# Kernel tuning notes

Measured on AMD Instinct MI355X. Metric: run time of the kernel, lower is better.

Reference implementation:

```python
import jax, jax.numpy as jnp
import numpy as np

B, S, H, M, E = 64, 512, 1024, 26, 676  # batch, seq, hidden, max_nodes, max_edges (M*M)


def setup_inputs() -> dict:
    key = jax.random.key(0)
    ks = jax.random.split(key, 16)
    seq = jax.random.normal(ks[0], (B, S, H), jnp.float32)
    # ragged, strictly-increasing sentence-end offsets in [1, S-1], zero-padded tail
    rng = np.random.RandomState(0)
    off = np.zeros((B, M - 1), np.int64)
    for b in range(B):
        c = rng.randint(5, M)  # count of valid offsets per sample (ragged)
        off[b, :c] = np.sort(rng.choice(np.arange(1, S), size=c, replace=False))
    s = 1.0 / np.sqrt(H)
    s3 = 1.0 / np.sqrt(3 * H)
    return {
        'sequence_outputs': seq,
        'proof_offsets': jnp.asarray(off),
        'node_labels': jax.random.randint(ks[1], (B, M), 0, 2),
        'edge_labels': jax.random.randint(ks[2], (B, E), 0, 2),
        'W_naf': jax.random.normal(ks[3], (H, H), jnp.float32) * s,
        'b_naf': jnp.zeros((H,), jnp.float32),
        'W_cd': jax.random.normal(ks[4], (H, H), jnp.float32) * s,
        'b_cd': jnp.zeros((H,), jnp.float32),
        'W_co': jax.random.normal(ks[5], (H, 2), jnp.float32) * s,
        'b_co': jnp.zeros((2,), jnp.float32),
        'W_nd': jax.random.normal(ks[6], (H, H), jnp.float32) * s,
        'b_nd': jnp.zeros((H,), jnp.float32),
        'W_no': jax.random.normal(ks[7], (H, 2), jnp.float32) * s,
        'b_no': jnp.zeros((2,), jnp.float32),
        'W_ed': jax.random.normal(ks[8], (3 * H, H), jnp.float32) * s3,
        'b_ed': jnp.zeros((H,), jnp.float32),
        'W_eo': jax.random.normal(ks[9], (H, 2), jnp.float32) * s,
        'b_eo': jnp.zeros((2,), jnp.float32),
    }


def reference(sequence_outputs, proof_offsets, node_labels, edge_labels,
              W_naf, b_naf, W_cd, b_cd, W_co, b_co,
              W_nd, b_nd, W_no, b_no, W_ed, b_ed, W_eo, b_eo):
    Bx, Sx, Hx = sequence_outputs.shape
    Mx = node_labels.shape[1]
    Ex = edge_labels.shape[1]

    cls = sequence_outputs[:, 0, :]                       # [B,H]
    naf = cls @ W_naf + b_naf                             # NAF node embedding
    logits = jnp.tanh(cls @ W_cd + b_cd) @ W_co + b_co    # RobertaClassificationHead (eval: dropout=id)

    # segment-mean pooling via inclusive prefix sums: segment j = tokens (prev_j, off_j]
    P = jnp.cumsum(sequence_outputs, axis=1)              # [B,S,H]
    off = proof_offsets                                   # [B,M-1]
    prev = jnp.concatenate([jnp.zeros((Bx, 1), off.dtype), off[:, :-1]], axis=1)
    valid = off > 0                                       # [B,M-1]
    seg_sum = (jnp.take_along_axis(P, off[..., None], axis=1)
               - jnp.take_along_axis(P, prev[..., None], axis=1))  # [B,M-1,H]
    seg_len = jnp.maximum(off - prev, 1).astype(sequence_outputs.dtype)
    seg_mean = seg_sum / seg_len[..., None] * valid[..., None]

    count = valid.sum(axis=1)                             # nodes per sample (excl. NAF)
    # node embeddings: seg means at 0..count-1, NAF at index count, zeros after
    node_full = jnp.concatenate([seg_mean, jnp.zeros((Bx, 1, Hx), seg_mean.dtype)], axis=1)  # [B,M,H]
    idx = jnp.arange(Mx)
    node_full = node_full + (idx[None, :, None] == count[:, None, None]) * naf[:, None, :]

    # all-pairs edge features over n=count+1 nodes, row-major flat k=i*n+j, zero-padded to E
    n = count + 1                                         # [B]
    k = jnp.arange(Ex)                                    # [E]
    i = jnp.clip(k[None, :] // n[:, None], 0, Mx - 1)     # [B,E]
    j = jnp.clip(k[None, :] % n[:, None], 0, Mx - 1)
    valid_e = (k[None, :] < (n * n)[:, None])[..., None]
    ni = jnp.take_along_axis(node_full, i[..., None], axis=1)  # [B,E,H]
    nj = jnp.take_along_axis(node_full, j[..., None], axis=1)
    edge = jnp.concatenate([nj, ni, nj - ni], axis=-1) * valid_e  # [B,E,3H]

    node_logits = jnp.tanh(node_full @ W_nd + b_nd) @ W_no + b_no
    edge_logits = jnp.tanh(edge @ W_ed + b_ed) @ W_eo + b_eo
    return (logits, node_logits, edge_logits)
```

## Files before the change

### kernel.cpp

```cpp
#include <hip/hip_runtime.h>
#include <hip/hip_bf16.h>

#define B_ 64
#define S_ 512
#define H_ 1024
#define M_ 26
#define E_ 676

typedef short bf16x8 __attribute__((ext_vector_type(8)));
typedef float f32x4 __attribute__((ext_vector_type(4)));

__device__ __forceinline__ void gload16(const void* g, void* l) {
    __builtin_amdgcn_global_load_lds((const __attribute__((address_space(1))) unsigned int*)g,
                                     (__attribute__((address_space(3))) unsigned int*)l,
                                     16, 0, 0);
}

__device__ __forceinline__ float tanh_fast(float x) {
    float e = __expf(2.0f * x);
    return 1.0f - 2.0f * __builtin_amdgcn_rcpf(e + 1.0f);
}

__global__ __launch_bounds__(256) void k_seg(
    const float* __restrict__ seq, const int* __restrict__ off,
    float* __restrict__ node_sum) {
    __shared__ float rows[8 * 1024];
    __shared__ int offs[26];
    __shared__ int cs[2];
    int bid = blockIdx.x;
    int tid = threadIdx.x;
    int chunk = bid & 63, b = bid >> 6;
    int t0 = chunk * 8;
    int wid = tid >> 6;

    const float* sq = seq + (size_t)b * S_ * H_ + (size_t)t0 * H_ + tid * 4;
    float* ld = rows + wid * 256;
#pragma unroll
    for (int i = 0; i < 8; ++i)
        gload16(sq + i * H_, ld + i * 1024);

    if (tid < M_ - 1) offs[tid] = off[b * (M_ - 1) + tid];
    __syncthreads();
    if (tid == 0) {
        int c = 0;
        while (c < M_ - 1 && offs[c] > 0) c++;
        cs[0] = c; cs[1] = (c > 0) ? offs[c - 1] : 0;
    }
    __syncthreads();
    int c = cs[0], offmax = cs[1];
    int ts = max(t0, 1), te = min(t0 + 7, offmax);
    if (ts > te) return;
    int m = 0;
    while (m < c && offs[m] < ts) m++;
    float4 acc = make_float4(0, 0, 0, 0);
#pragma unroll
    for (int i = 0; i < 8; ++i) {
        int t = t0 + i;
        if (t < ts || t > te) continue;
        if (offs[m] < t) {
            float* dst = node_sum + ((size_t)(b * M_ + m)) * H_ + tid * 4;
            atomicAdd(dst + 0, acc.x); atomicAdd(dst + 1, acc.y);
            atomicAdd(dst + 2, acc.z); atomicAdd(dst + 3, acc.w);
            acc = make_float4(0, 0, 0, 0);
            while (offs[m] < t) m++;
        }
        float4 v = *(const float4*)(rows + i * 1024 + tid * 4);
        acc.x += v.x; acc.y += v.y; acc.z += v.z; acc.w += v.w;
    }
    float* dst = node_sum + ((size_t)(b * M_ + m)) * H_ + tid * 4;
    atomicAdd(dst + 0, acc.x); atomicAdd(dst + 1, acc.y);
    atomicAdd(dst + 2, acc.z); atomicAdd(dst + 3, acc.w);
}

__global__ __launch_bounds__(256) void k_stage1b(
    const float* __restrict__ seq, const int* __restrict__ off,
    const float* __restrict__ Wnaf, const float* __restrict__ Wcd,
    const float* __restrict__ Wnd, const float* __restrict__ Wed,
    const float* __restrict__ bed, const float* __restrict__ Weo,
    const float* __restrict__ beo,
    __hip_bfloat16* __restrict__ Wt, int* __restrict__ count,
    float* __restrict__ econ, float* __restrict__ naf, float* __restrict__ cdh) {
    __shared__ float smem[2048];
    int bid = blockIdx.x;
    int tid = threadIdx.x;

    if (bid < 256) {
        float (*As)[64] = (float(*)[64])smem;
        float (*Bs)[64] = (float(*)[64])(smem + 1024);
        int e = bid;
        int bx = e & 31;
        int kbase = (e >> 5) * 128;
        const float* W;
        float* dst;
        int cbase;
        if (bx < 16) { W = Wnaf; dst = naf; cbase = bx * 64; }
        else         { W = Wcd;  dst = cdh; cbase = (bx - 16) * 64; }
        int tx = tid % 16, ty = tid / 16;
        float c[4][4] = {};
        int la_row = tid / 4;
        int la_k4  = (tid % 4) * 4;
        int lb_k   = tid / 16;
        int lb_c4  = (tid % 16) * 4;
        for (int k0 = 0; k0 < 128; k0 += 16) {
            float4 a = *(const float4*)(seq + (size_t)la_row * S_ * H_ + kbase + k0 + la_k4);
            *(float4*)(&Bs[lb_k][lb_c4]) =
                *(const float4*)(W + (size_t)(kbase + k0 + lb_k) * H_ + cbase + lb_c4);
            As[la_k4 + 0][la_row] = a.x;
            As[la_k4 + 1][la_row] = a.y;
            As[la_k4 + 2][la_row] = a.z;
            As[la_k4 + 3][la_row] = a.w;
            __syncthreads();
#pragma unroll
            for (int kk = 0; kk < 16; ++kk) {
                float4 av = *(const float4*)(&As[kk][ty * 4]);
                float4 bv = *(const float4*)(&Bs[kk][tx * 4]);
                c[0][0] += av.x * bv.x; c[0][1] += av.x * bv.y; c[0][2] += av.x * bv.z; c[0][3] += av.x * bv.w;
                c[1][0] += av.y * bv.x; c[1][1] += av.y * bv.y; c[1][2] += av.y * bv.z; c[1][3] += av.y * bv.w;
                c[2][0] += av.z * bv.x; c[2][1] += av.z * bv.y; c[2][2] += av.z * bv.z; c[2][3] += av.z * bv.w;
                c[3][0] += av.w * bv.x; c[3][1] += av.w * bv.y; c[3][2] += av.w * bv.z; c[3][3] += av.w * bv.w;
            }
            __syncthreads();
        }
#pragma unroll
        for (int i = 0; i < 4; ++i)
#pragma unroll
            for (int j = 0; j < 4; ++j)
                atomicAdd(dst + (size_t)(ty * 4 + i) * H_ + cbase + tx * 4 + j, c[i][j]);
    } else if (bid < 3328) {
        float (*T)[33] = (float(*)[33])smem;
        int idx = bid - 256;
        int s = idx >> 10, rem = idx & 1023;
        int bx = rem & 31, by = rem >> 5;
        int c = tid & 31, r0 = tid >> 5;
        const int HH = H_ * H_;
#pragma unroll
        for (int i = 0; i < 4; ++i) {
            int r = r0 + 8 * i;
            size_t k = by * 32 + r, n = bx * 32 + c;
            float v;
            if (s == 0)      v = Wnd[k * H_ + n];
            else if (s == 1) v = Wed[k * H_ + n] + Wed[2 * HH + k * H_ + n];
            else             v = Wed[HH + k * H_ + n] - Wed[2 * HH + k * H_ + n];
            T[r][c] = v;
        }
        __syncthreads();
#pragma unroll
        for (int i = 0; i < 4; ++i) {
            int rr = r0 + 8 * i;
            Wt[(size_t)(s * H_ + bx * 32 + rr) * H_ + by * 32 + c] = __float2bfloat16(T[c][rr]);
        }
    } else if (bid == 3328) {
        if (tid < 64) {
            int b = tid;
            int c = 0;
            for (int m = 0; m < M_ - 1; ++m) c += (off[b * (M_ - 1) + m] > 0) ? 1 : 0;
            count[b] = c;
        }
    } else {
        float* s0 = smem; float* s1 = smem + 256;
        float a0 = 0.f, a1 = 0.f;
        for (int h = tid; h < H_; h += 256) {
            float t = tanh_fast(bed[h]);
            a0 += t * Weo[h * 2 + 0];
            a1 += t * Weo[h * 2 + 1];
        }
        s0[tid] = a0; s1[tid] = a1; __syncthreads();
        for (int o = 128; o > 0; o >>= 1) {
            if (tid < o) { s0[tid] += s0[tid + o]; s1[tid] += s1[tid + o]; }
            __syncthreads();
        }
        if (tid == 0) { econ[0] = s0[0] + beo[0]; econ[1] = s1[0] + beo[1]; }
    }
}

__global__ __launch_bounds__(256) void k_stage2(
    const float* __restrict__ sums, const int* __restrict__ off,
    const int* __restrict__ count, const float* __restrict__ naf,
    const float* __restrict__ bnaf, __hip_bfloat16* __restrict__ nodeB,
    const float* __restrict__ cdh, const float* __restrict__ bcd,
    const float* __restrict__ Wco, const float* __restrict__ bco,
    float* __restrict__ out) {
    __shared__ float smem[512];
    int bid = blockIdx.x;
    int tid = threadIdx.x;
    if (bid < 1664) {
        int b = bid / 26, m = bid - b * 26;
        int cnt = count[b];
        float4 v = make_float4(0, 0, 0, 0);
        const float4* row = (const float4*)(sums + ((size_t)(b * M_ + m)) * H_);
        if (m < M_ - 1) {
            int o = off[b * (M_ - 1) + m];
            if (o > 0) {
                int prev = (m > 0) ? off[b * (M_ - 1) + m - 1] : 0;
                float inv = 1.0f / (float)max(o - prev, 1);
                float4 s = row[tid];
                v = make_float4(s.x * inv, s.y * inv, s.z * inv, s.w * inv);
            }
        }
        if (m == cnt) {
            float4 a = ((const float4*)(naf + (size_t)b * H_))[tid];
            float4 bb = ((const float4*)bnaf)[tid];
            v.x += a.x + bb.x; v.y += a.y + bb.y; v.z += a.z + bb.z; v.w += a.w + bb.w;
        }
        __hip_bfloat16 __attribute__((aligned(8))) h[4] = {
            __float2bfloat16(v.x), __float2bfloat16(v.y),
            __float2bfloat16(v.z), __float2bfloat16(v.w)};
        *(ushort4*)(nodeB + ((size_t)(b * M_ + m)) * H_ + tid * 4) = *(const ushort4*)h;
    } else {
        int b = bid - 1664;
        float* s0 = smem; float* s1 = smem + 256;
        float a0 = 0.f, a1 = 0.f;
        for (int h = tid; h < H_; h += 256) {
            float t = tanh_fast(cdh[(size_t)b * H_ + h] + bcd[h]);
            a0 += t * Wco[h * 2 + 0];
            a1 += t * Wco[h * 2 + 1];
        }
        s0[tid] = a0; s1[tid] = a1; __syncthreads();
        for (int o = 128; o > 0; o >>= 1) {
            if (tid < o) { s0[tid] += s0[tid + o]; s1[tid] += s1[tid + o]; }
            __syncthreads();
        }
        if (tid == 0) { out[b * 2 + 0] = s0[0] + bco[0]; out[b * 2 + 1] = s1[0] + bco[1]; }
    }
}

#define GM 1664
#define GN 3072
#define GK 1024
__global__ __launch_bounds__(256) void k_mfma(const __hip_bfloat16* __restrict__ A,
                                              const __hip_bfloat16* __restrict__ Bt,
                                              float* __restrict__ C) {
    __shared__ __hip_bfloat16 As[128 * 32];
    __shared__ __hip_bfloat16 Bs[128 * 32];
    int tid = threadIdx.x;
    int wid = tid >> 6, ln = tid & 63;
    int row0 = blockIdx.y * 128, col0 = blockIdx.x * 128;
    const __hip_bfloat16* ga = A + (size_t)(row0 + wid * 16 + (ln >> 2)) * GK + (ln & 3) * 8;
    const __hip_bfloat16* gb = Bt + (size_t)(col0 + wid * 16 + (ln >> 2)) * GK + (ln & 3) * 8;
    __hip_bfloat16* lA = As + wid * 512;
    __hip_bfloat16* lB = Bs + wid * 512;
    int mrow = (wid >> 1) * 64, ncol = (wid & 1) * 64;
    int l15 = ln & 15, l4 = ln >> 4;
    f32x4 acc[4][4] = {};
    const __hip_bfloat16* pa = As + (size_t)(mrow + l15) * 32 + l4 * 8;
    const __hip_bfloat16* pb = Bs + (size_t)(ncol + l15) * 32 + l4 * 8;
    for (int k0 = 0; k0 < GK; k0 += 32) {
        gload16(ga, lA);
        gload16(ga + 64 * GK, lA + 2048);
        gload16(gb, lB);
        gload16(gb + 64 * GK, lB + 2048);
        ga += 32; gb += 32;
        __syncthreads();
        bf16x8 af[4], bf[4];
#pragma unroll
        for (int mi = 0; mi < 4; ++mi) af[mi] = *(const bf16x8*)(pa + mi * 16 * 32);
#pragma unroll
        for (int ni = 0; ni < 4; ++ni) bf[ni] = *(const bf16x8*)(pb + ni * 16 * 32);
#pragma unroll
        for (int mi = 0; mi < 4; ++mi)
#pragma unroll
            for (int ni = 0; ni < 4; ++ni)
                acc[mi][ni] = __builtin_amdgcn_mfma_f32_16x16x32_bf16(af[mi], bf[ni],
                                                                      acc[mi][ni], 0, 0, 0);
        __syncthreads();
    }
#pragma unroll
    for (int mi = 0; mi < 4; ++mi)
#pragma unroll
        for (int ni = 0; ni < 4; ++ni) {
            f32x4 v = acc[mi][ni];
            size_t r = row0 + mrow + mi * 16 + l4 * 4;
            size_t cc = col0 + ncol + ni * 16 + l15;
            C[(r + 0) * GN + cc] = v[0];
            C[(r + 1) * GN + cc] = v[1];
            C[(r + 2) * GN + cc] = v[2];
            C[(r + 3) * GN + cc] = v[3];
        }
}

__global__ __launch_bounds__(256) void k_stage4(
    const float* __restrict__ Cm, const int* __restrict__ count,
    const float* __restrict__ bnd, const float* __restrict__ Wno,
    const float* __restrict__ bno, const float* __restrict__ bed,
    const float* __restrict__ Weo, const float* __restrict__ beo,
    const float* __restrict__ econ, float* __restrict__ out_n,
    float* __restrict__ out_e) {
    int bid = blockIdx.x;
    int wid = threadIdx.x >> 6, lane = threadIdx.x & 63;
    if (bid < 416) {
        int r = bid * 4 + wid;
        const float4* src = (const float4*)(Cm + (size_t)r * GN);
        float a0 = 0.f, a1 = 0.f;
#pragma unroll
        for (int it = 0; it < 4; ++it) {
            int h = lane * 4 + it * 256;
            float4 s = src[lane + it * 64];
            float4 bb = *(const float4*)(bnd + h);
            float t0 = tanh_fast(s.x + bb.x), t1 = tanh_fast(s.y + bb.y);
            float t2 = tanh_fast(s.z + bb.z), t3 = tanh_fast(s.w + bb.w);
            a0 += t0 * Wno[h * 2 + 0] + t1 * Wno[h * 2 + 2] + t2 * Wno[h * 2 + 4] + t3 * Wno[h * 2 + 6];
            a1 += t0 * Wno[h * 2 + 1] + t1 * Wno[h * 2 + 3] + t2 * Wno[h * 2 + 5] + t3 * Wno[h * 2 + 7];
        }
        for (int o = 32; o > 0; o >>= 1) { a0 += __shfl_down(a0, o); a1 += __shfl_down(a1, o); }
        if (lane == 0) { out_n[(size_t)r * 2 + 0] = a0 + bno[0]; out_n[(size_t)r * 2 + 1] = a1 + bno[1]; }
    } else {
        int e = bid - 416;
        int b = e >> 4;
        int wg = (e & 15) * 4 + wid;
        int n = count[b] + 1;
        int n2 = n * n;
        float4 bed4[4], w04[4], w14[4];
#pragma unroll
        for (int it = 0; it < 4; ++it) {
            int h = lane * 4 + it * 256;
            bed4[it] = *(const float4*)(bed + h);
            w04[it] = make_float4(Weo[h * 2 + 0], Weo[h * 2 + 2], Weo[h * 2 + 4], Weo[h * 2 + 6]);
            w14[it] = make_float4(Weo[h * 2 + 1], Weo[h * 2 + 3], Weo[h * 2 + 5], Weo[h * 2 + 7]);
        }
        float e0 = econ[0], e1 = econ[1];
        float b0 = beo[0], b1 = beo[1];
        for (int k = wg; k < E_; k += 64) {
            float* dst = out_e + ((size_t)b * E_ + k) * 2;
            if (k >= n2) {
                if (lane == 0) { dst[0] = e0; dst[1] = e1; }
                continue;
            }
            int i = k / n, j = k - i * n;
            const float4* U4 = (const float4*)(Cm + (size_t)(b * M_ + j) * GN + H_);
            const float4* V4 = (const float4*)(Cm + (size_t)(b * M_ + i) * GN + 2 * H_);
            float a0 = 0.f, a1 = 0.f;
#pragma unroll
            for (int it = 0; it < 4; ++it) {
                float4 u = U4[lane + it * 64];
                float4 v = V4[lane + it * 64];
                float t0 = tanh_fast(u.x + v.x + bed4[it].x);
                float t1 = tanh_fast(u.y + v.y + bed4[it].y);
                float t2 = tanh_fast(u.z + v.z + bed4[it].z);
                float t3 = tanh_fast(u.w + v.w + bed4[it].w);
                a0 += t0 * w04[it].x + t1 * w04[it].y + t2 * w04[it].z + t3 * w04[it].w;
                a1 += t0 * w14[it].x + t1 * w14[it].y + t2 * w14[it].z + t3 * w14[it].w;
            }
            for (int o = 32; o > 0; o >>= 1) { a0 += __shfl_down(a0, o); a1 += __shfl_down(a1, o); }
            if (lane == 0) { dst[0] = a0 + b0; dst[1] = a1 + b1; }
        }
    }
}

extern "C" void kernel_launch(void* const* d_in, const int* in_sizes, int n_in,
                              void* d_out, int out_size, void* d_ws, size_t ws_size,
                              hipStream_t stream) {
    const float* seq  = (const float*)d_in[0];
    const int*   off  = (const int*)d_in[1];
    const float* Wnaf = (const float*)d_in[4];  const float* bnaf = (const float*)d_in[5];
    const float* Wcd  = (const float*)d_in[6];  const float* bcd  = (const float*)d_in[7];
    const float* Wco  = (const float*)d_in[8];  const float* bco  = (const float*)d_in[9];
    const float* Wnd  = (const float*)d_in[10]; const float* bnd  = (const float*)d_in[11];
    const float* Wno  = (const float*)d_in[12]; const float* bno  = (const float*)d_in[13];
    const float* Wed  = (const float*)d_in[14]; const float* bed  = (const float*)d_in[15];
    const float* Weo  = (const float*)d_in[16]; const float* beo  = (const float*)d_in[17];
    float* out = (float*)d_out;

    float* ws = (float*)d_ws;
    size_t p = 0;
    float* nodeS = ws + p;  p += (size_t)B_ * M_ * H_;
    float* naf   = ws + p;  p += (size_t)B_ * H_;
    float* cdh   = ws + p;  p += (size_t)B_ * H_;
    __hip_bfloat16* nodeB = (__hip_bfloat16*)(ws + p); p += (size_t)B_ * M_ * H_ / 2;
    __hip_bfloat16* Wt    = (__hip_bfloat16*)(ws + p); p += (size_t)3 * H_ * H_ / 2;
    float* Cbuf  = ws + p;  p += (size_t)B_ * M_ * 3 * H_;
    int*   cnt   = (int*)(ws + p); p += 64;
    float* econ  = ws + p;  p += 2;

    hipMemsetAsync(nodeS, 0, ((size_t)B_ * M_ * H_ + 2 * (size_t)B_ * H_) * sizeof(float),
                   stream);

    k_seg<<<dim3(4096), 256, 0, stream>>>(seq, off, nodeS);
    k_stage1b<<<dim3(3330), 256, 0, stream>>>(seq, off, Wnaf, Wcd, Wnd, Wed, bed, Weo, beo,
                                              Wt, cnt, econ, naf, cdh);
    k_stage2<<<dim3(1728), 256, 0, stream>>>(nodeS, off, cnt, naf, bnaf, nodeB,
                                             cdh, bcd, Wco, bco, out);
    k_mfma<<<dim3(GN / 128, GM / 128), 256, 0, stream>>>(nodeB, Wt, Cbuf);
    k_stage4<<<dim3(1440), 256, 0, stream>>>(Cbuf, cnt, bnd, Wno, bno, bed, Weo, beo, econ,
                                             out + B_ * 2, out + B_ * 2 + B_ * M_ * 2);
}
```

Measured before the change: 349.0 us.

## Rewrite segment pooling as per-sample sequential scan with pipelined LDS prefetch

The segment-sum kernel now uses one block per (sample, quarter of hidden) that walks tokens sequentially through a 4-deep ring of async global-to-LDS loads, writing each segment sum directly instead of using atomics. This removes the float atomics and the large memset of the node-sum buffer, since the kernel zeroes unused rows itself, and it reads only tokens up to the last offset. In exchange the grid drops from 4096 to 256 blocks, so each block's serial token walk sets latency and parallelism is lower.

```diff
diff --git a/kernel.cpp b/kernel.cpp
--- a/kernel.cpp
+++ b/kernel.cpp
@@ -24,52 +24,84 @@
 __global__ __launch_bounds__(256) void k_seg(
     const float* __restrict__ seq, const int* __restrict__ off,
     float* __restrict__ node_sum) {
-    __shared__ float rows[8 * 1024];
-    __shared__ int offs[26];
-    __shared__ int cs[2];
+    __shared__ float buf[4][16 * 256];
+    __shared__ int offs_s[32];
     int bid = blockIdx.x;
     int tid = threadIdx.x;
-    int chunk = bid & 63, b = bid >> 6;
-    int t0 = chunk * 8;
-    int wid = tid >> 6;
-
-    const float* sq = seq + (size_t)b * S_ * H_ + (size_t)t0 * H_ + tid * 4;
-    float* ld = rows + wid * 256;
-#pragma unroll
-    for (int i = 0; i < 8; ++i)
-        gload16(sq + i * H_, ld + i * 1024);
-
-    if (tid < M_ - 1) offs[tid] = off[b * (M_ - 1) + tid];
+    int b = bid >> 2, hs = bid & 3;
+    int w = tid >> 6;
+    int lane4 = (tid & 63) * 4;
+
+    if (tid < M_ - 1) offs_s[tid] = off[b * (M_ - 1) + tid];
     __syncthreads();
-    if (tid == 0) {
-        int c = 0;
-        while (c < M_ - 1 && offs[c] > 0) c++;
-        cs[0] = c; cs[1] = (c > 0) ? offs[c - 1] : 0;
-    }
-    __syncthreads();
-    int c = cs[0], offmax = cs[1];
-    int ts = max(t0, 1), te = min(t0 + 7, offmax);
-    if (ts > te) return;
+
+    int c = 0;
+    while (c < M_ - 1 && offs_s[c] > 0) c++;
+    int offmax = offs_s[c - 1];
+    int nt = (offmax + 15) >> 4;
+
+    float* ns_base = node_sum + ((size_t)b * M_) * H_ + hs * 256 + tid;
+    for (int m = c; m < M_; ++m) ns_base[(size_t)m * H_] = 0.f;
+
+    const float* src0 = seq + (size_t)b * S_ * H_ + hs * 256;
+#pragma unroll
+    for (int j0 = 0; j0 < 4; ++j0) {
+#pragma unroll
+        for (int i = 0; i < 4; ++i) {
+            int r = 4 * w + i;
+            int t = 1 + 16 * j0 + r; t = min(t, 511);
+            gload16(src0 + (size_t)t * H_ + lane4, &buf[j0][r * 256]);
+        }
+    }
+
     int m = 0;
-    while (m < c && offs[m] < ts) m++;
-    float4 acc = make_float4(0, 0, 0, 0);
-#pragma unroll
-    for (int i = 0; i < 8; ++i) {
-        int t = t0 + i;
-        if (t < ts || t > te) continue;
-        if (offs[m] < t) {
-            float* dst = node_sum + ((size_t)(b * M_ + m)) * H_ + tid * 4;
-            atomicAdd(dst + 0, acc.x); atomicAdd(dst + 1, acc.y);
-            atomicAdd(dst + 2, acc.z); atomicAdd(dst + 3, acc.w);
-            acc = make_float4(0, 0, 0, 0);
-            while (offs[m] < t) m++;
-        }
-        float4 v = *(const float4*)(rows + i * 1024 + tid * 4);
-        acc.x += v.x; acc.y += v.y; acc.z += v.z; acc.w += v.w;
-    }
-    float* dst = node_sum + ((size_t)(b * M_ + m)) * H_ + tid * 4;
-    atomicAdd(dst + 0, acc.x); atomicAdd(dst + 1, acc.y);
-    atomicAdd(dst + 2, acc.z); atomicAdd(dst + 3, acc.w);
+    int cur = offs_s[0];
+    float acc = 0.f;
+    int ntc = (nt > 4) ? nt : 4;
+    for (int j = 0; j < nt; ++j) {
+        int ahead = ntc - 1 - j; ahead = (ahead > 3) ? 3 : ahead;
+        if (ahead == 3)      asm volatile("s_waitcnt vmcnt(12)" ::: "memory");
+        else if (ahead == 2) asm volatile("s_waitcnt vmcnt(8)" ::: "memory");
+        else if (ahead == 1) asm volatile("s_waitcnt vmcnt(4)" ::: "memory");
+        else                 asm volatile("s_waitcnt vmcnt(0)" ::: "memory");
+        __builtin_amdgcn_s_barrier();
+
+        const float* bj = &buf[j & 3][0];
+        int tbase = 1 + 16 * j;
+        if (tbase + 15 <= offmax) {
+#pragma unroll
+            for (int r = 0; r < 16; ++r) {
+                int t = tbase + r;
+                acc += bj[r * 256 + tid];
+                if (t == cur) {
+                    ns_base[(size_t)m * H_] = acc;
+                    acc = 0.f; ++m;
+                    cur = (m < c) ? offs_s[m] : 0x7fffffff;
+                }
+            }
+        } else {
+            for (int r = 0; r < 16; ++r) {
+                int t = tbase + r;
+                if (t > offmax) break;
+                acc += bj[r * 256 + tid];
+                if (t == cur) {
+                    ns_base[(size_t)m * H_] = acc;
+                    acc = 0.f; ++m;
+                    cur = (m < c) ? offs_s[m] : 0x7fffffff;
+                }
+            }
+        }
+        __builtin_amdgcn_s_barrier();
+        if (j + 4 < nt) {
+#pragma unroll
+            for (int i = 0; i < 4; ++i) {
+                int r = 4 * w + i;
+                int t = 1 + 16 * (j + 4) + r; t = min(t, 511);
+                gload16(src0 + (size_t)t * H_ + lane4, &buf[j & 3][r * 256]);
+            }
+        }
+    }
+    asm volatile("s_waitcnt vmcnt(0)" ::: "memory");
 }
 
 __global__ __launch_bounds__(256) void k_stage1b(
@@ -371,10 +403,9 @@
     int*   cnt   = (int*)(ws + p); p += 64;
     float* econ  = ws + p;  p += 2;
 
-    hipMemsetAsync(nodeS, 0, ((size_t)B_ * M_ * H_ + 2 * (size_t)B_ * H_) * sizeof(float),
-                   stream);
-
-    k_seg<<<dim3(4096), 256, 0, stream>>>(seq, off, nodeS);
+    hipMemsetAsync(naf, 0, 2 * (size_t)B_ * H_ * sizeof(float), stream);
+
+    k_seg<<<dim3(256), 256, 0, stream>>>(seq, off, nodeS);
     k_stage1b<<<dim3(3330), 256, 0, stream>>>(seq, off, Wnaf, Wcd, Wnd, Wed, bed, Weo, beo,
                                               Wt, cnt, econ, naf, cdh);
     k_stage2<<<dim3(1728), 256, 0, stream>>>(nodeS, off, cnt, naf, bnaf, nodeB,
```

After: 327.4 us. 1.07x faster.
